# Kernel optimization log

Hardware: AMD Instinct MI355X
Metric: run time of the kernel (lower is better)

Reference implementation:

```python
import jax, jax.numpy as jnp
import numpy as np

N_NODES = 100000
N_EDGES = 1250000
D = 64


def setup_inputs() -> dict:
    key = jax.random.key(0)
    k0, k1, k2, k3, k4 = jax.random.split(key, 5)
    feat = jax.random.normal(k0, (N_NODES, D), dtype=jnp.float32)
    src = jax.random.randint(k1, (N_EDGES,), 0, N_NODES)
    dst = jax.random.randint(k2, (N_EDGES,), 0, N_NODES)
    # GIN apply_func: Linear(D, D) -> ReLU -> Linear(D, D)
    scale = 1.0 / np.sqrt(D)
    W1 = jax.random.uniform(k3, (D, D), dtype=jnp.float32, minval=-scale, maxval=scale)
    b1 = jnp.zeros((D,), dtype=jnp.float32)
    W2 = jax.random.uniform(k4, (D, D), dtype=jnp.float32, minval=-scale, maxval=scale)
    b2 = jnp.zeros((D,), dtype=jnp.float32)
    eps = jnp.zeros((1,), dtype=jnp.float32)  # learnable eps, init 0
    return {"feat": feat, "W1": W1, "b1": b1, "W2": W2, "b2": b2,
            "eps": eps, "src": src, "dst": dst}


def reference(feat, W1, b1, W2, b2, eps, src, dst):
    # copy_u + sum reduce: gather source features per edge, scatter-add to dst
    msgs = feat[src]                                   # [E, D]
    neigh = jax.ops.segment_sum(msgs, dst, num_segments=feat.shape[0])  # [N, D]
    rst = (1.0 + eps) * feat + neigh                   # combine
    # apply_func (f_Theta): 2-layer MLP
    h = jax.nn.relu(rst @ W1 + b1)
    out = h @ W2 + b2
    return out
```

## Files before the change

kernel.cpp:

```cpp
#include <hip/hip_runtime.h>
#include <hip/hip_bf16.h>

#define N_NODES 100000
#define N_EDGES 1250000
#define DIM 64
#define NB 782
#define NCHUNK 512
#define CHUNK 2442
#define MAXE 4096

typedef __attribute__((ext_vector_type(8))) short short8;
typedef __attribute__((ext_vector_type(8))) __bf16 bf16x8;
typedef __attribute__((ext_vector_type(4))) float f32x4;

static __device__ __forceinline__ short f2bf(float f) {
    union { float f; unsigned u; } v; v.f = f;
    unsigned r = (v.u + 0x7fffu + ((v.u >> 16) & 1u)) >> 16;
    return (short)r;
}
static __device__ __forceinline__ float bfu2f(unsigned u) {
    union { unsigned u; float f; } v; v.u = u << 16; return v.f;
}

__global__ __launch_bounds__(256) void prologue(const float* __restrict__ feat,
                                                short* __restrict__ featbf,
                                                const float* __restrict__ W1,
                                                const float* __restrict__ W2,
                                                short* __restrict__ wf,
                                                int basePrep) {
    int blk = blockIdx.x;
    if (blk < basePrep) {
        int i = (blk * 256 + threadIdx.x) * 8;
        float4 a = *(const float4*)(feat + i);
        float4 b = *(const float4*)(feat + i + 4);
        short8 t;
        t[0] = f2bf(a.x); t[1] = f2bf(a.y); t[2] = f2bf(a.z); t[3] = f2bf(a.w);
        t[4] = f2bf(b.x); t[5] = f2bf(b.y); t[6] = f2bf(b.z); t[7] = f2bf(b.w);
        *(short8*)(featbf + i) = t;
    } else {
        int idx = (blk - basePrep) * 256 + threadIdx.x;
        int layer = idx >> 12;
        int fi = idx & 4095;
        int fragidx = fi >> 9;
        int lane = (fi >> 3) & 63;
        int jj = fi & 7;
        int ct = fragidx >> 1, kt = fragidx & 1;
        int k = kt * 32 + (lane >> 4) * 8 + jj;
        int j = ct * 16 + (lane & 15);
        const float* W = layer ? W2 : W1;
        wf[idx] = f2bf(W[k * DIM + j]);
    }
}

__global__ __launch_bounds__(512) void partition3(const int* __restrict__ src,
                                                  const int* __restrict__ dst,
                                                  int* __restrict__ offs_g,
                                                  int* __restrict__ edgebuf) {
    __shared__ int cnt[NB];
    __shared__ int lcur[NB];
    __shared__ int partial[512];
    __shared__ int estage[CHUNK];

    int c = blockIdx.x;
    int t = threadIdx.x;
    int base = c * CHUNK;
    int end = base + CHUNK; if (end > N_EDGES) end = N_EDGES;

    for (int b = t; b < NB; b += 512) cnt[b] = 0;
    __syncthreads();
    for (int i = base + t; i < end; i += 512)
        atomicAdd(&cnt[dst[i] >> 7], 1);
    __syncthreads();

    int b0 = 2 * t, b1 = 2 * t + 1;
    int v0 = (b0 < NB) ? cnt[b0] : 0;
    int v1 = (b1 < NB) ? cnt[b1] : 0;
    partial[t] = v0 + v1;
    __syncthreads();
    for (int off = 1; off < 512; off <<= 1) {
        int u = (t >= off) ? partial[t - off] : 0;
        __syncthreads();
        partial[t] += u;
        __syncthreads();
    }
    int ex = partial[t] - (v0 + v1);
    int* orow = offs_g + (size_t)c * (NB + 1);
    if (b0 < NB) { lcur[b0] = ex;      orow[b0] = ex; }
    if (b1 < NB) { lcur[b1] = ex + v0; orow[b1] = ex + v0; }
    if (t == 511) orow[NB] = partial[511];
    __syncthreads();

    for (int i = base + t; i < end; i += 512) {
        int d = dst[i];
        int p = atomicAdd(&lcur[d >> 7], 1);
        estage[p] = src[i] | ((d & 127) << 17);
    }
    __syncthreads();

    int n = end - base;
    for (int i = t; i < n; i += 512) edgebuf[base + i] = estage[i];
}

template<int BF>
__global__ __launch_bounds__(512) void fused_gather_mlp(const int* __restrict__ offs_g,
                                                        const int* __restrict__ edgebuf,
                                                        const void* __restrict__ featp,
                                                        const float* __restrict__ feat,
                                                        const short* __restrict__ wf,
                                                        const float* __restrict__ b1,
                                                        const float* __restrict__ b2,
                                                        const float* __restrict__ epsp,
                                                        float* __restrict__ out) {
    __shared__ union {
        struct { int ew[MAXE]; int es[MAXE]; } s;
        float tile[128][66];
    } u;
    __shared__ int cnt[128], offs[128], cur[128];
    __shared__ int slen[NCHUNK], dloc[NCHUNK];
    __shared__ int sh_ec;

    int b = blockIdx.x;
    int node0 = b << 7;
    int tid = threadIdx.x;
    int c = tid & 15;
    int slot = tid >> 4;

    const int* row = offs_g + (size_t)tid * (NB + 1);
    int s0 = row[b];
    int myslen = row[b + 1] - s0;
    dloc[tid] = myslen;
    __syncthreads();
    for (int off = 1; off < 512; off <<= 1) {
        int v = (tid >= off) ? dloc[tid - off] : 0;
        __syncthreads();
        dloc[tid] += v;
        __syncthreads();
    }
    int incl = dloc[tid];
    __syncthreads();
    dloc[tid] = incl - myslen;
    slen[tid] = myslen;
    if (tid == 511) sh_ec = incl;
    __syncthreads();
    int ec = sh_ec;

    float acc[4][4];
#pragma unroll
    for (int g = 0; g < 4; ++g)
#pragma unroll
        for (int j = 0; j < 4; ++j) acc[g][j] = 0.f;

    int c0 = 0;
    while (c0 < NCHUNK) {
        int rbase = dloc[c0];
        int pred = (tid >= c0) && (dloc[tid] + slen[tid] - rbase <= MAXE);
        int nc = __syncthreads_count(pred);
        int c1 = c0 + nc;

        if (tid < 128) cnt[tid] = 0;
        if (tid >= c0 && tid < c1 && myslen > 0) {
            int d0 = dloc[tid] - rbase;
            const int* sp = edgebuf + (size_t)tid * CHUNK + s0;
            for (int i = 0; i < myslen; ++i) u.s.ew[d0 + i] = sp[i];
        }
        __syncthreads();

        int n = ((c1 < NCHUNK) ? dloc[c1] : ec) - rbase;

        for (int i = tid; i < n; i += 512)
            atomicAdd(&cnt[(u.s.ew[i] >> 17) & 127], 1);
        __syncthreads();

        if (tid < 128) offs[tid] = cnt[tid];
        __syncthreads();
        for (int d = 1; d < 128; d <<= 1) {
            int v = 0;
            if (tid < 128 && tid >= d) v = offs[tid - d];
            __syncthreads();
            if (tid < 128 && tid >= d) offs[tid] += v;
            __syncthreads();
        }
        if (tid < 128) {
            int x = offs[tid] - cnt[tid];
            offs[tid] = x;
            cur[tid] = x;
        }
        __syncthreads();

        for (int i = tid; i < n; i += 512) {
            int w = u.s.ew[i];
            int p = atomicAdd(&cur[(w >> 17) & 127], 1);
            u.s.es[p] = w & 0x1FFFF;
        }
        __syncthreads();

#pragma unroll
        for (int g = 0; g < 4; ++g) {
            int ld = g * 32 + slot;
            int e0 = offs[ld], e1 = e0 + cnt[ld];
            int i = e0;
            for (; i + 1 < e1; i += 2) {
                int sa = u.s.es[i], sb = u.s.es[i + 1];
                if (BF) {
                    uint2 pa = ((const uint2*)featp)[sa * 16 + c];
                    uint2 pb = ((const uint2*)featp)[sb * 16 + c];
                    acc[g][0] += bfu2f(pa.x & 0xffffu) + bfu2f(pb.x & 0xffffu);
                    acc[g][1] += bfu2f(pa.x >> 16)     + bfu2f(pb.x >> 16);
                    acc[g][2] += bfu2f(pa.y & 0xffffu) + bfu2f(pb.y & 0xffffu);
                    acc[g][3] += bfu2f(pa.y >> 16)     + bfu2f(pb.y >> 16);
                } else {
                    float4 va = ((const float4*)featp)[sa * 16 + c];
                    float4 vb = ((const float4*)featp)[sb * 16 + c];
                    acc[g][0] += va.x + vb.x;
                    acc[g][1] += va.y + vb.y;
                    acc[g][2] += va.z + vb.z;
                    acc[g][3] += va.w + vb.w;
                }
            }
            if (i < e1) {
                int sa = u.s.es[i];
                if (BF) {
                    uint2 pa = ((const uint2*)featp)[sa * 16 + c];
                    acc[g][0] += bfu2f(pa.x & 0xffffu);
                    acc[g][1] += bfu2f(pa.x >> 16);
                    acc[g][2] += bfu2f(pa.y & 0xffffu);
                    acc[g][3] += bfu2f(pa.y >> 16);
                } else {
                    float4 va = ((const float4*)featp)[sa * 16 + c];
                    acc[g][0] += va.x; acc[g][1] += va.y;
                    acc[g][2] += va.z; acc[g][3] += va.w;
                }
            }
        }
        __syncthreads();
        c0 = c1;
    }

#pragma unroll
    for (int g = 0; g < 4; ++g) {
        int ld = g * 32 + slot;
#pragma unroll
        for (int j = 0; j < 4; ++j)
            u.tile[ld][c * 4 + j] = acc[g][j];
    }
    __syncthreads();

    int wv = tid >> 6;
    int lane = tid & 63;
    int r = lane & 15, gg = lane >> 4;
    int lrow = wv * 16 + r;
    int node = node0 + lrow;
    bool valid = node < N_NODES;
    float epsv = 1.0f + epsp[0];

    const short8* w1f8 = (const short8*)(wf);
    const short8* w2f8 = (const short8*)(wf + 4096);

    short8 a[2];
    {
        const float* fp = feat + (size_t)node * 64 + gg * 8;
#pragma unroll
        for (int kt = 0; kt < 2; ++kt) {
            float f0x=0,f0y=0,f0z=0,f0w=0,f1x=0,f1y=0,f1z=0,f1w=0;
            if (valid) {
                float4 f0 = *(const float4*)(fp + kt * 32);
                float4 f1 = *(const float4*)(fp + kt * 32 + 4);
                f0x=f0.x; f0y=f0.y; f0z=f0.z; f0w=f0.w;
                f1x=f1.x; f1y=f1.y; f1z=f1.z; f1w=f1.w;
            }
            const float2* tp = (const float2*)&u.tile[lrow][kt * 32 + gg * 8];
            float2 n0 = tp[0], n1 = tp[1], n2 = tp[2], n3 = tp[3];
            float rs[8] = { epsv * f0x + n0.x, epsv * f0y + n0.y,
                            epsv * f0z + n1.x, epsv * f0w + n1.y,
                            epsv * f1x + n2.x, epsv * f1y + n2.y,
                            epsv * f1z + n3.x, epsv * f1w + n3.y };
            short8 t;
#pragma unroll
            for (int jj = 0; jj < 8; ++jj) t[jj] = f2bf(rs[jj]);
            a[kt] = t;
        }
    }
    __syncthreads();

    f32x4 acc1[4];
#pragma unroll
    for (int ct = 0; ct < 4; ++ct) {
        float bv = b1[ct * 16 + r];
        f32x4 cc = { bv, bv, bv, bv };
        cc = __builtin_amdgcn_mfma_f32_16x16x32_bf16(
                __builtin_bit_cast(bf16x8, a[0]),
                __builtin_bit_cast(bf16x8, w1f8[(ct * 2 + 0) * 64 + lane]),
                cc, 0, 0, 0);
        cc = __builtin_amdgcn_mfma_f32_16x16x32_bf16(
                __builtin_bit_cast(bf16x8, a[1]),
                __builtin_bit_cast(bf16x8, w1f8[(ct * 2 + 1) * 64 + lane]),
                cc, 0, 0, 0);
        acc1[ct] = cc;
    }

#pragma unroll
    for (int ct = 0; ct < 4; ++ct)
#pragma unroll
        for (int i = 0; i < 4; ++i)
            u.tile[wv * 16 + gg * 4 + i][ct * 16 + r] = fmaxf(acc1[ct][i], 0.0f);
    __syncthreads();

    short8 a2[2];
#pragma unroll
    for (int kt = 0; kt < 2; ++kt) {
        const float2* hp = (const float2*)&u.tile[wv * 16 + r][kt * 32 + gg * 8];
        float2 h0 = hp[0], h1 = hp[1], h2 = hp[2], h3 = hp[3];
        float hs[8] = { h0.x, h0.y, h1.x, h1.y, h2.x, h2.y, h3.x, h3.y };
        short8 t;
#pragma unroll
        for (int jj = 0; jj < 8; ++jj) t[jj] = f2bf(hs[jj]);
        a2[kt] = t;
    }

    f32x4 acc2[4];
#pragma unroll
    for (int ct = 0; ct < 4; ++ct) {
        float bv = b2[ct * 16 + r];
        f32x4 cc = { bv, bv, bv, bv };
        cc = __builtin_amdgcn_mfma_f32_16x16x32_bf16(
                __builtin_bit_cast(bf16x8, a2[0]),
                __builtin_bit_cast(bf16x8, w2f8[(ct * 2 + 0) * 64 + lane]),
                cc, 0, 0, 0);
        cc = __builtin_amdgcn_mfma_f32_16x16x32_bf16(
                __builtin_bit_cast(bf16x8, a2[1]),
                __builtin_bit_cast(bf16x8, w2f8[(ct * 2 + 1) * 64 + lane]),
                cc, 0, 0, 0);
        acc2[ct] = cc;
    }

#pragma unroll
    for (int ct = 0; ct < 4; ++ct)
#pragma unroll
        for (int i = 0; i < 4; ++i) {
            int nrow = node0 + wv * 16 + gg * 4 + i;
            if (nrow < N_NODES)
                out[(size_t)nrow * 64 + ct * 16 + r] = acc2[ct][i];
        }
}

__global__ __launch_bounds__(256) void scatter_edges(const float4* __restrict__ feat4,
                                                     const int* __restrict__ src,
                                                     const int* __restrict__ dst,
                                                     float* __restrict__ neigh) {
    int idx = blockIdx.x * 256 + threadIdx.x;
    int e = idx >> 4, c = idx & 15;
    int s = src[e], d = dst[e];
    float4 v = feat4[s * 16 + c];
    float* p = neigh + d * 64 + c * 4;
    unsafeAtomicAdd(p + 0, v.x);
    unsafeAtomicAdd(p + 1, v.y);
    unsafeAtomicAdd(p + 2, v.z);
    unsafeAtomicAdd(p + 3, v.w);
}

__global__ __launch_bounds__(256) void prep_w(const float* __restrict__ W1,
                                              const float* __restrict__ W2,
                                              short* __restrict__ wf) {
    int idx = blockIdx.x * 256 + threadIdx.x;
    int layer = idx >> 12;
    int fi = idx & 4095;
    int fragidx = fi >> 9;
    int lane = (fi >> 3) & 63;
    int jj = fi & 7;
    int ct = fragidx >> 1, kt = fragidx & 1;
    int k = kt * 32 + (lane >> 4) * 8 + jj;
    int j = ct * 16 + (lane & 15);
    const float* W = layer ? W2 : W1;
    wf[idx] = f2bf(W[k * DIM + j]);
}

__global__ __launch_bounds__(256) void gin_mlp(const float* __restrict__ feat,
                                               float* __restrict__ neigh_out,
                                               const short* __restrict__ wf,
                                               const float* __restrict__ b1,
                                               const float* __restrict__ b2,
                                               const float* __restrict__ epsp) {
    __shared__ float hbuf[4][16][66];
    int lane = threadIdx.x & 63;
    int wv = threadIdx.x >> 6;
    int r = lane & 15, g = lane >> 4;
    int row0 = blockIdx.x * 64 + wv * 16;
    int node = row0 + r;
    bool valid = node < N_NODES;
    float epsv = 1.0f + epsp[0];
    const short8* w1f8 = (const short8*)(wf);
    const short8* w2f8 = (const short8*)(wf + 4096);
    short8 a[2];
    if (valid) {
        const float* fp = feat + node * 64 + g * 8;
        const float* np_ = neigh_out + node * 64 + g * 8;
#pragma unroll
        for (int kt = 0; kt < 2; ++kt) {
            float4 f0 = *(const float4*)(fp + kt * 32);
            float4 f1 = *(const float4*)(fp + kt * 32 + 4);
            float4 n0 = *(const float4*)(np_ + kt * 32);
            float4 n1 = *(const float4*)(np_ + kt * 32 + 4);
            float rs[8] = { epsv * f0.x + n0.x, epsv * f0.y + n0.y,
                            epsv * f0.z + n0.z, epsv * f0.w + n0.w,
                            epsv * f1.x + n1.x, epsv * f1.y + n1.y,
                            epsv * f1.z + n1.z, epsv * f1.w + n1.w };
            short8 t;
#pragma unroll
            for (int jj = 0; jj < 8; ++jj) t[jj] = f2bf(rs[jj]);
            a[kt] = t;
        }
    } else {
        short8 z = { 0,0,0,0,0,0,0,0 };
        a[0] = z; a[1] = z;
    }
    f32x4 acc[4];
#pragma unroll
    for (int ct = 0; ct < 4; ++ct) {
        float bv = b1[ct * 16 + r];
        f32x4 c = { bv, bv, bv, bv };
        c = __builtin_amdgcn_mfma_f32_16x16x32_bf16(
                __builtin_bit_cast(bf16x8, a[0]),
                __builtin_bit_cast(bf16x8, w1f8[(ct * 2 + 0) * 64 + lane]), c, 0, 0, 0);
        c = __builtin_amdgcn_mfma_f32_16x16x32_bf16(
                __builtin_bit_cast(bf16x8, a[1]),
                __builtin_bit_cast(bf16x8, w1f8[(ct * 2 + 1) * 64 + lane]), c, 0, 0, 0);
        acc[ct] = c;
    }
#pragma unroll
    for (int ct = 0; ct < 4; ++ct)
#pragma unroll
        for (int i = 0; i < 4; ++i)
            hbuf[wv][g * 4 + i][ct * 16 + r] = fmaxf(acc[ct][i], 0.0f);
    __syncthreads();
    short8 a2[2];
#pragma unroll
    for (int kt = 0; kt < 2; ++kt) {
        const float2* hp = (const float2*)&hbuf[wv][r][kt * 32 + g * 8];
        float2 h0 = hp[0], h1 = hp[1], h2 = hp[2], h3 = hp[3];
        float hs[8] = { h0.x, h0.y, h1.x, h1.y, h2.x, h2.y, h3.x, h3.y };
        short8 t;
#pragma unroll
        for (int jj = 0; jj < 8; ++jj) t[jj] = f2bf(hs[jj]);
        a2[kt] = t;
    }
    f32x4 acc2[4];
#pragma unroll
    for (int ct = 0; ct < 4; ++ct) {
        float bv = b2[ct * 16 + r];
        f32x4 c = { bv, bv, bv, bv };
        c = __builtin_amdgcn_mfma_f32_16x16x32_bf16(
                __builtin_bit_cast(bf16x8, a2[0]),
                __builtin_bit_cast(bf16x8, w2f8[(ct * 2 + 0) * 64 + lane]), c, 0, 0, 0);
        c = __builtin_amdgcn_mfma_f32_16x16x32_bf16(
                __builtin_bit_cast(bf16x8, a2[1]),
                __builtin_bit_cast(bf16x8, w2f8[(ct * 2 + 1) * 64 + lane]), c, 0, 0, 0);
        acc2[ct] = c;
    }
#pragma unroll
    for (int ct = 0; ct < 4; ++ct)
#pragma unroll
        for (int i = 0; i < 4; ++i) {
            int nrow = row0 + g * 4 + i;
            if (nrow < N_NODES)
                neigh_out[nrow * 64 + ct * 16 + r] = acc2[ct][i];
        }
}

extern "C" void kernel_launch(void* const* d_in, const int* in_sizes, int n_in,
                              void* d_out, int out_size, void* d_ws, size_t ws_size,
                              hipStream_t stream) {
    const float* feat = (const float*)d_in[0];
    const float* W1   = (const float*)d_in[1];
    const float* b1   = (const float*)d_in[2];
    const float* W2   = (const float*)d_in[3];
    const float* b2   = (const float*)d_in[4];
    const float* eps  = (const float*)d_in[5];
    const int*   src  = (const int*)d_in[6];
    const int*   dst  = (const int*)d_in[7];
    float* out = (float*)d_out;

    char* ws = (char*)d_ws;
    short* wf = (short*)ws;

    const size_t featbf_bytes = (size_t)N_NODES * DIM * 2;
    const size_t offs_bytes   = (size_t)NCHUNK * (NB + 1) * 4;
    const size_t edge_bytes   = (size_t)NCHUNK * CHUNK * 4;
    const size_t need_mid  = 16384 + offs_bytes + edge_bytes;
    const size_t need_full = need_mid + featbf_bytes;

    if (ws_size >= need_mid) {
        char* p = ws + 16384;
        short* featbf = nullptr;
        if (ws_size >= need_full) { featbf = (short*)p; p += featbf_bytes; }
        int* offs_g  = (int*)p;            p += offs_bytes;
        int* edgebuf = (int*)p;

        int basePrep = featbf ? 3125 : 0;
        prologue<<<basePrep + 32, 256, 0, stream>>>(feat, featbf, W1, W2, wf, basePrep);

        partition3<<<NCHUNK, 512, 0, stream>>>(src, dst, offs_g, edgebuf);

        if (featbf)
            fused_gather_mlp<1><<<NB, 512, 0, stream>>>(
                offs_g, edgebuf, featbf, feat, wf, b1, b2, eps, out);
        else
            fused_gather_mlp<0><<<NB, 512, 0, stream>>>(
                offs_g, edgebuf, feat, feat, wf, b1, b2, eps, out);
    } else {
        prep_w<<<32, 256, 0, stream>>>(W1, W2, wf);
        hipMemsetAsync(d_out, 0, (size_t)N_NODES * DIM * sizeof(float), stream);
        scatter_edges<<<(N_EDGES * 16) / 256, 256, 0, stream>>>(
            (const float4*)feat, src, dst, out);
        gin_mlp<<<(N_NODES + 63) / 64, 256, 0, stream>>>(feat, out, wf, b1, b2, eps);
    }
}
```

Before: 63.16 us.

## Transpose chunk offsets, interleave four node gathers, read self features as bf16

The per-chunk bucket offsets are stored transposed so the gather kernel's 512 threads read consecutive addresses for a bucket instead of strided rows. The edge gather loop now walks all four destination nodes of a thread in lockstep, issuing up to four independent loads per iteration to raise memory-level parallelism. The self-feature term in the MLP stage reads the bf16 copy instead of fp32, halving those bytes but adding bf16 rounding to the (1+eps)*feat term. Lockstep iteration costs predicated work when the four nodes have uneven degree, and partition3's offset writes become strided.

```diff
diff --git a/kernel.cpp b/kernel.cpp
--- a/kernel.cpp
+++ b/kernel.cpp
@@ -20,6 +20,9 @@
 }
 static __device__ __forceinline__ float bfu2f(unsigned u) {
     union { unsigned u; float f; } v; v.u = u << 16; return v.f;
+}
+static __device__ __forceinline__ float bfs2f(short s) {
+    union { unsigned u; float f; } v; v.u = ((unsigned)(unsigned short)s) << 16; return v.f;
 }
 
 __global__ __launch_bounds__(256) void prologue(const float* __restrict__ feat,
@@ -54,7 +57,7 @@
 
 __global__ __launch_bounds__(512) void partition3(const int* __restrict__ src,
                                                   const int* __restrict__ dst,
-                                                  int* __restrict__ offs_g,
+                                                  int* __restrict__ offs_gT,
                                                   int* __restrict__ edgebuf) {
     __shared__ int cnt[NB];
     __shared__ int lcur[NB];
@@ -84,10 +87,9 @@
         __syncthreads();
     }
     int ex = partial[t] - (v0 + v1);
-    int* orow = offs_g + (size_t)c * (NB + 1);
-    if (b0 < NB) { lcur[b0] = ex;      orow[b0] = ex; }
-    if (b1 < NB) { lcur[b1] = ex + v0; orow[b1] = ex + v0; }
-    if (t == 511) orow[NB] = partial[511];
+    if (b0 < NB) { lcur[b0] = ex;      offs_gT[(size_t)b0 * NCHUNK + c] = ex; }
+    if (b1 < NB) { lcur[b1] = ex + v0; offs_gT[(size_t)b1 * NCHUNK + c] = ex + v0; }
+    if (t == 511) offs_gT[(size_t)NB * NCHUNK + c] = partial[511];
     __syncthreads();
 
     for (int i = base + t; i < end; i += 512) {
@@ -102,7 +104,7 @@
 }
 
 template<int BF>
-__global__ __launch_bounds__(512) void fused_gather_mlp(const int* __restrict__ offs_g,
+__global__ __launch_bounds__(512) void fused_gather_mlp(const int* __restrict__ offs_gT,
                                                         const int* __restrict__ edgebuf,
                                                         const void* __restrict__ featp,
                                                         const float* __restrict__ feat,
@@ -125,9 +127,8 @@
     int c = tid & 15;
     int slot = tid >> 4;
 
-    const int* row = offs_g + (size_t)tid * (NB + 1);
-    int s0 = row[b];
-    int myslen = row[b + 1] - s0;
+    int s0 = offs_gT[(size_t)b * NCHUNK + tid];
+    int myslen = offs_gT[(size_t)(b + 1) * NCHUNK + tid] - s0;
     dloc[tid] = myslen;
     __syncthreads();
     for (int off = 1; off < 512; off <<= 1) {
@@ -194,42 +195,51 @@
         }
         __syncthreads();
 
+        int b_[4], n_[4], mx = 0;
 #pragma unroll
         for (int g = 0; g < 4; ++g) {
             int ld = g * 32 + slot;
-            int e0 = offs[ld], e1 = e0 + cnt[ld];
-            int i = e0;
-            for (; i + 1 < e1; i += 2) {
-                int sa = u.s.es[i], sb = u.s.es[i + 1];
-                if (BF) {
-                    uint2 pa = ((const uint2*)featp)[sa * 16 + c];
-                    uint2 pb = ((const uint2*)featp)[sb * 16 + c];
-                    acc[g][0] += bfu2f(pa.x & 0xffffu) + bfu2f(pb.x & 0xffffu);
-                    acc[g][1] += bfu2f(pa.x >> 16)     + bfu2f(pb.x >> 16);
-                    acc[g][2] += bfu2f(pa.y & 0xffffu) + bfu2f(pb.y & 0xffffu);
-                    acc[g][3] += bfu2f(pa.y >> 16)     + bfu2f(pb.y >> 16);
-                } else {
-                    float4 va = ((const float4*)featp)[sa * 16 + c];
-                    float4 vb = ((const float4*)featp)[sb * 16 + c];
-                    acc[g][0] += va.x + vb.x;
-                    acc[g][1] += va.y + vb.y;
-                    acc[g][2] += va.z + vb.z;
-                    acc[g][3] += va.w + vb.w;
+            b_[g] = offs[ld];
+            n_[g] = cnt[ld];
+            mx = n_[g] > mx ? n_[g] : mx;
+        }
+        for (int it = 0; it < mx; ++it) {
+            if (BF) {
+                uint2 p0, p1, p2, p3;
+                bool v0 = it < n_[0], v1 = it < n_[1], v2 = it < n_[2], v3 = it < n_[3];
+                const uint2* fb = (const uint2*)featp;
+                if (v0) p0 = fb[u.s.es[b_[0] + it] * 16 + c];
+                if (v1) p1 = fb[u.s.es[b_[1] + it] * 16 + c];
+                if (v2) p2 = fb[u.s.es[b_[2] + it] * 16 + c];
+                if (v3) p3 = fb[u.s.es[b_[3] + it] * 16 + c];
+                if (v0) {
+                    acc[0][0] += bfu2f(p0.x & 0xffffu); acc[0][1] += bfu2f(p0.x >> 16);
+                    acc[0][2] += bfu2f(p0.y & 0xffffu); acc[0][3] += bfu2f(p0.y >> 16);
                 }
-            }
-            if (i < e1) {
-                int sa = u.s.es[i];
-                if (BF) {
-                    uint2 pa = ((const uint2*)featp)[sa * 16 + c];
-                    acc[g][0] += bfu2f(pa.x & 0xffffu);
-                    acc[g][1] += bfu2f(pa.x >> 16);
-                    acc[g][2] += bfu2f(pa.y & 0xffffu);
-                    acc[g][3] += bfu2f(pa.y >> 16);
-                } else {
-                    float4 va = ((const float4*)featp)[sa * 16 + c];
-                    acc[g][0] += va.x; acc[g][1] += va.y;
-                    acc[g][2] += va.z; acc[g][3] += va.w;
+                if (v1) {
+                    acc[1][0] += bfu2f(p1.x & 0xffffu); acc[1][1] += bfu2f(p1.x >> 16);
+                    acc[1][2] += bfu2f(p1.y & 0xffffu); acc[1][3] += bfu2f(p1.y >> 16);
                 }
+                if (v2) {
+                    acc[2][0] += bfu2f(p2.x & 0xffffu); acc[2][1] += bfu2f(p2.x >> 16);
+                    acc[2][2] += bfu2f(p2.y & 0xffffu); acc[2][3] += bfu2f(p2.y >> 16);
+                }
+                if (v3) {
+                    acc[3][0] += bfu2f(p3.x & 0xffffu); acc[3][1] += bfu2f(p3.x >> 16);
+                    acc[3][2] += bfu2f(p3.y & 0xffffu); acc[3][3] += bfu2f(p3.y >> 16);
+                }
+            } else {
+                float4 q0, q1, q2, q3;
+                bool v0 = it < n_[0], v1 = it < n_[1], v2 = it < n_[2], v3 = it < n_[3];
+                const float4* ff = (const float4*)featp;
+                if (v0) q0 = ff[u.s.es[b_[0] + it] * 16 + c];
+                if (v1) q1 = ff[u.s.es[b_[1] + it] * 16 + c];
+                if (v2) q2 = ff[u.s.es[b_[2] + it] * 16 + c];
+                if (v3) q3 = ff[u.s.es[b_[3] + it] * 16 + c];
+                if (v0) { acc[0][0] += q0.x; acc[0][1] += q0.y; acc[0][2] += q0.z; acc[0][3] += q0.w; }
+                if (v1) { acc[1][0] += q1.x; acc[1][1] += q1.y; acc[1][2] += q1.z; acc[1][3] += q1.w; }
+                if (v2) { acc[2][0] += q2.x; acc[2][1] += q2.y; acc[2][2] += q2.z; acc[2][3] += q2.w; }
+                if (v3) { acc[3][0] += q3.x; acc[3][1] += q3.y; acc[3][2] += q3.z; acc[3][3] += q3.w; }
             }
         }
         __syncthreads();
@@ -257,28 +267,34 @@
     const short8* w2f8 = (const short8*)(wf + 4096);
 
     short8 a[2];
-    {
-        const float* fp = feat + (size_t)node * 64 + gg * 8;
-#pragma unroll
-        for (int kt = 0; kt < 2; ++kt) {
-            float f0x=0,f0y=0,f0z=0,f0w=0,f1x=0,f1y=0,f1z=0,f1w=0;
+#pragma unroll
+    for (int kt = 0; kt < 2; ++kt) {
+        float fv[8];
+        if (BF) {
+            short8 f8 = { 0,0,0,0,0,0,0,0 };
+            if (valid) f8 = ((const short8*)featp)[node * 8 + kt * 4 + gg];
+#pragma unroll
+            for (int jj = 0; jj < 8; ++jj) fv[jj] = bfs2f(f8[jj]);
+        } else {
+            float4 f0 = { 0,0,0,0 }, f1 = { 0,0,0,0 };
             if (valid) {
-                float4 f0 = *(const float4*)(fp + kt * 32);
-                float4 f1 = *(const float4*)(fp + kt * 32 + 4);
-                f0x=f0.x; f0y=f0.y; f0z=f0.z; f0w=f0.w;
-                f1x=f1.x; f1y=f1.y; f1z=f1.z; f1w=f1.w;
+                const float* fp = feat + (size_t)node * 64 + kt * 32 + gg * 8;
+                f0 = *(const float4*)fp;
+                f1 = *(const float4*)(fp + 4);
             }
-            const float2* tp = (const float2*)&u.tile[lrow][kt * 32 + gg * 8];
-            float2 n0 = tp[0], n1 = tp[1], n2 = tp[2], n3 = tp[3];
-            float rs[8] = { epsv * f0x + n0.x, epsv * f0y + n0.y,
-                            epsv * f0z + n1.x, epsv * f0w + n1.y,
-                            epsv * f1x + n2.x, epsv * f1y + n2.y,
-                            epsv * f1z + n3.x, epsv * f1w + n3.y };
-            short8 t;
-#pragma unroll
-            for (int jj = 0; jj < 8; ++jj) t[jj] = f2bf(rs[jj]);
-            a[kt] = t;
-        }
+            fv[0]=f0.x; fv[1]=f0.y; fv[2]=f0.z; fv[3]=f0.w;
+            fv[4]=f1.x; fv[5]=f1.y; fv[6]=f1.z; fv[7]=f1.w;
+        }
+        const float2* tp = (const float2*)&u.tile[lrow][kt * 32 + gg * 8];
+        float2 n0 = tp[0], n1 = tp[1], n2 = tp[2], n3 = tp[3];
+        float rs[8] = { epsv * fv[0] + n0.x, epsv * fv[1] + n0.y,
+                        epsv * fv[2] + n1.x, epsv * fv[3] + n1.y,
+                        epsv * fv[4] + n2.x, epsv * fv[5] + n2.y,
+                        epsv * fv[6] + n3.x, epsv * fv[7] + n3.y };
+        short8 t;
+#pragma unroll
+        for (int jj = 0; jj < 8; ++jj) t[jj] = f2bf(rs[jj]);
+        a[kt] = t;
     }
     __syncthreads();
 
@@ -483,7 +499,7 @@
     short* wf = (short*)ws;
 
     const size_t featbf_bytes = (size_t)N_NODES * DIM * 2;
-    const size_t offs_bytes   = (size_t)NCHUNK * (NB + 1) * 4;
+    const size_t offs_bytes   = (size_t)(NB + 1) * NCHUNK * 4;
     const size_t edge_bytes   = (size_t)NCHUNK * CHUNK * 4;
     const size_t need_mid  = 16384 + offs_bytes + edge_bytes;
     const size_t need_full = need_mid + featbf_bytes;
@@ -492,20 +508,20 @@
         char* p = ws + 16384;
         short* featbf = nullptr;
         if (ws_size >= need_full) { featbf = (short*)p; p += featbf_bytes; }
-        int* offs_g  = (int*)p;            p += offs_bytes;
+        int* offs_gT = (int*)p;            p += offs_bytes;
         int* edgebuf = (int*)p;
 
         int basePrep = featbf ? 3125 : 0;
         prologue<<<basePrep + 32, 256, 0, stream>>>(feat, featbf, W1, W2, wf, basePrep);
 
-        partition3<<<NCHUNK, 512, 0, stream>>>(src, dst, offs_g, edgebuf);
+        partition3<<<NCHUNK, 512, 0, stream>>>(src, dst, offs_gT, edgebuf);
 
         if (featbf)
             fused_gather_mlp<1><<<NB, 512, 0, stream>>>(
-                offs_g, edgebuf, featbf, feat, wf, b1, b2, eps, out);
+                offs_gT, edgebuf, featbf, feat, wf, b1, b2, eps, out);
         else
             fused_gather_mlp<0><<<NB, 512, 0, stream>>>(
-                offs_g, edgebuf, feat, feat, wf, b1, b2, eps, out);
+                offs_gT, edgebuf, feat, feat, wf, b1, b2, eps, out);
     } else {
         prep_w<<<32, 256, 0, stream>>>(W1, W2, wf);
         hipMemsetAsync(d_out, 0, (size_t)N_NODES * DIM * sizeof(float), stream);
```

Result: slower. 103.4 us (+63.7%).
